# Kernel tuning notes

Hardware: AMD Instinct MI355X
Metric: run time of the kernel (lower is better)

The kernel has to match this reference:

```python
import jax, jax.numpy as jnp
import numpy as np

# ---- config (mirrors cfg / init kwargs) ----
FEAT_STRIDE = 16
IM_DIMS = (1024, 1024)          # (height, width)
ANCHOR_SCALES = (8, 16, 32)
ANCHOR_RATIOS = (0.5, 1.0, 2.0)
PRE_NMS_TOPN = 6000             # eval mode (cfg_key=1)
POST_NMS_TOPN = 300
NMS_THRESH = 0.7
MIN_SIZE = 16


def _generate_base_anchors(base_size=16, ratios=ANCHOR_RATIOS, scales=ANCHOR_SCALES):
    """py-faster-rcnn generate_anchors, in numpy (static)."""
    def mk(ws, hs, xc, yc):
        return np.stack([xc - 0.5 * (ws - 1), yc - 0.5 * (hs - 1),
                         xc + 0.5 * (ws - 1), yc + 0.5 * (hs - 1)], axis=1)
    base = np.array([0, 0, base_size - 1, base_size - 1], dtype=np.float64)
    w = base[2] - base[0] + 1; h = base[3] - base[1] + 1
    xc = base[0] + 0.5 * (w - 1); yc = base[1] + 0.5 * (h - 1)
    # ratio enum
    size = w * h
    ws = np.round(np.sqrt(size / np.array(ratios)))
    hs = np.round(ws * np.array(ratios))
    ratio_anchors = mk(ws, hs, xc, yc)
    # scale enum
    out = []
    for a in ratio_anchors:
        aw = a[2] - a[0] + 1; ah = a[3] - a[1] + 1
        axc = a[0] + 0.5 * (aw - 1); ayc = a[1] + 0.5 * (ah - 1)
        out.append(mk(aw * np.array(scales), ah * np.array(scales), axc, ayc))
    return np.concatenate(out, axis=0).astype(np.float32)  # [A,4]


def _all_anchors(H, W):
    base = _generate_base_anchors()                       # [A,4]
    sx = np.arange(W) * FEAT_STRIDE
    sy = np.arange(H) * FEAT_STRIDE
    sx, sy = np.meshgrid(sx, sy)
    shifts = np.stack([sx.ravel(), sy.ravel(), sx.ravel(), sy.ravel()], axis=1)  # [H*W,4]
    anchors = shifts[:, None, :].astype(np.float32) + base[None, :, :]
    return anchors.reshape(-1, 4)                         # [H*W*A, 4]


def setup_inputs() -> dict:
    key = jax.random.key(0)
    k1, k2 = jax.random.split(key)
    H, W, A = 64, 64, 9
    rpn_cls_score = jax.random.normal(k1, (1, H, W, 2 * A), dtype=jnp.float32)
    rpn_bbox_pred = jax.random.normal(k2, (1, H, W, 4 * A), dtype=jnp.float32)
    return {"rpn_cls_score": rpn_cls_score, "rpn_bbox_pred": rpn_bbox_pred}


def _proposals(rpn_cls_score, rpn_bbox_pred):
    _, H, W, C2 = rpn_cls_score.shape
    A = C2 // 2
    # rpn_softmax: per-anchor 2-way softmax, foreground prob
    scores = jax.nn.softmax(rpn_cls_score.reshape(H, W, A, 2), axis=-1)[..., 1].reshape(-1)  # [N]
    deltas = rpn_bbox_pred.reshape(-1, 4)                  # [N,4]
    anchors = jnp.asarray(_all_anchors(H, W))              # [N,4]
    # bbox_transform_inv
    aw = anchors[:, 2] - anchors[:, 0] + 1.0
    ah = anchors[:, 3] - anchors[:, 1] + 1.0
    axc = anchors[:, 0] + 0.5 * aw
    ayc = anchors[:, 1] + 0.5 * ah
    dx, dy, dw, dh = deltas[:, 0], deltas[:, 1], deltas[:, 2], deltas[:, 3]
    pxc = dx * aw + axc; pyc = dy * ah + ayc
    pw = jnp.exp(dw) * aw; ph = jnp.exp(dh) * ah
    x1 = pxc - 0.5 * pw; y1 = pyc - 0.5 * ph
    x2 = pxc + 0.5 * pw; y2 = pyc + 0.5 * ph
    # clip to image
    im_h, im_w = IM_DIMS
    x1 = jnp.clip(x1, 0.0, im_w - 1.0); x2 = jnp.clip(x2, 0.0, im_w - 1.0)
    y1 = jnp.clip(y1, 0.0, im_h - 1.0); y2 = jnp.clip(y2, 0.0, im_h - 1.0)
    boxes = jnp.stack([x1, y1, x2, y2], axis=1)            # [N,4]
    # filter too-small boxes by masking their score
    valid = ((x2 - x1 + 1.0) >= MIN_SIZE) & ((y2 - y1 + 1.0) >= MIN_SIZE)
    scores = jnp.where(valid, scores, -jnp.inf)
    return boxes, scores


def _nms_keep(boxes, K):
    """Greedy NMS keep-mask over score-descending boxes [K,4]."""
    x1, y1, x2, y2 = boxes[:, 0], boxes[:, 1], boxes[:, 2], boxes[:, 3]
    areas = (x2 - x1 + 1.0) * (y2 - y1 + 1.0)
    ix1 = jnp.maximum(x1[:, None], x1[None, :])
    iy1 = jnp.maximum(y1[:, None], y1[None, :])
    ix2 = jnp.minimum(x2[:, None], x2[None, :])
    iy2 = jnp.minimum(y2[:, None], y2[None, :])
    iw = jnp.maximum(ix2 - ix1 + 1.0, 0.0)
    ih = jnp.maximum(iy2 - iy1 + 1.0, 0.0)
    inter = iw * ih
    iou = inter / (areas[:, None] + areas[None, :] - inter)  # [K,K]
    idxs = jnp.arange(K)
    def body(i, keep):
        sup = keep[i] & (iou[i] > NMS_THRESH) & (idxs > i)
        return keep & ~sup
    return jax.lax.fori_loop(0, K, body, jnp.ones((K,), bool))


def reference(rpn_cls_score, rpn_bbox_pred):
    boxes, scores = _proposals(rpn_cls_score, rpn_bbox_pred)
    K = min(PRE_NMS_TOPN, scores.shape[0])
    top_scores, order = jax.lax.top_k(scores, K)           # score-descending
    top_boxes = boxes[order]                               # [K,4]
    keep = _nms_keep(top_boxes, K)
    sel_scores = jnp.where(keep, top_scores, -jnp.inf)
    _, idx = jax.lax.top_k(sel_scores, POST_NMS_TOPN)      # kept, in score order
    out_boxes = top_boxes[idx]                             # [post,4]
    blob = jnp.concatenate([jnp.zeros((POST_NMS_TOPN, 1), out_boxes.dtype), out_boxes], axis=1)
    return blob                                            # [post,5] (batch_idx, x1,y1,x2,y2)
```

## Files before the change

kernel.cpp:

```cpp
#include <hip/hip_runtime.h>
#include <stdint.h>

typedef unsigned long long u64;
typedef unsigned int u32;

#define N_ANCH 36864
#define WGRID 64
#define A_PER 9
#define KTOP 6000
#define NOUT 300
#define NBIN 5120
#define NCHK 94
#define NJ   6016
#define NSLOT 12
#define SPILLCAP 64
#define SCAP 6144

#define BARRIER_LDS() do {                                   \
    asm volatile("s_waitcnt lgkmcnt(0)" ::: "memory");       \
    __builtin_amdgcn_s_barrier();                            \
    asm volatile("" ::: "memory");                           \
} while (0)

__constant__ float c_ax1[9] = {-84.f,-176.f,-360.f,-56.f,-120.f,-248.f,-36.f,-80.f,-168.f};
__constant__ float c_ay1[9] = {-40.f,-88.f,-184.f,-56.f,-120.f,-248.f,-80.f,-168.f,-344.f};
__constant__ float c_aw[9]  = {184.f,368.f,736.f,128.f,256.f,512.f,88.f,176.f,352.f};
__constant__ float c_ah[9]  = {96.f,192.f,384.f,128.f,256.f,512.f,176.f,352.f,704.f};

__device__ __forceinline__ u32 binof(u32 u) {
    if (u < 0x80000000u) return 0u;
    if (u < 0xBF000000u) return 1u + ((u - 0x80000000u) >> 22);
    return 256u + ((u - 0xBF000000u) >> 11);
}

__device__ __forceinline__ bool iou_gt(float4 a, float areaA, float4 b, float areaB) {
    float ix1 = fmaxf(a.x, b.x), iy1 = fmaxf(a.y, b.y);
    float ix2 = fminf(a.z, b.z), iy2 = fminf(a.w, b.w);
    float iw = fmaxf(ix2 - ix1 + 1.0f, 0.0f);
    float ih = fmaxf(iy2 - iy1 + 1.0f, 0.0f);
    float inter = iw * ih;
    float iou = inter / (areaA + areaB - inter);
    return iou > 0.7f;
}

__global__ __launch_bounds__(256) void proposal_kernel(const float* __restrict__ cls,
                                                       const float* __restrict__ dlt,
                                                       u64* __restrict__ keys,
                                                       float4* __restrict__ boxes) {
    const int t = threadIdx.x;
    int i = blockIdx.x * 256 + t;
    int a  = i % A_PER;
    int hw = i / A_PER;
    int wx = hw % WGRID;
    int hy = hw / WGRID;

    float2 lp = *(const float2*)(cls + hw * 18 + 2 * a);
    float l0 = lp.x, l1 = lp.y;
    float m  = fmaxf(l0, l1);
    float e0 = expf(l0 - m), e1 = expf(l1 - m);
    float s  = e1 / (e0 + e1);

    float4 dd = *(const float4*)(dlt + hw * 36 + 4 * a);
    float dx = dd.x, dy = dd.y, dw = dd.z, dh = dd.w;
    float aw = c_aw[a], ah = c_ah[a];
    float axc = (c_ax1[a] + 16.f * (float)wx) + 0.5f * aw;
    float ayc = (c_ay1[a] + 16.f * (float)hy) + 0.5f * ah;

    float pxc = dx * aw + axc;
    float pyc = dy * ah + ayc;
    float pw  = expf(dw) * aw;
    float phh = expf(dh) * ah;
    float x1 = pxc - 0.5f * pw, y1 = pyc - 0.5f * phh;
    float x2 = pxc + 0.5f * pw, y2 = pyc + 0.5f * phh;
    x1 = fminf(fmaxf(x1, 0.f), 1023.f);
    x2 = fminf(fmaxf(x2, 0.f), 1023.f);
    y1 = fminf(fmaxf(y1, 0.f), 1023.f);
    y2 = fminf(fmaxf(y2, 0.f), 1023.f);
    bool valid = ((x2 - x1 + 1.f) >= 16.f) && ((y2 - y1 + 1.f) >= 16.f);
    float sc = valid ? s : -__builtin_huge_valf();

    u32 sb  = __float_as_uint(sc);
    u32 ord = (sb & 0x80000000u) ? ~sb : (sb | 0x80000000u);
    u64 key = ((u64)ord << 32) | (u32)(~(u32)i);
    keys[i]  = key;
    boxes[i] = make_float4(x1, y1, x2, y2);
}

__global__ __launch_bounds__(1024) void select_kernel(const u64* __restrict__ keys,
                                                      const float4* __restrict__ boxes,
                                                      u64* __restrict__ gscat,
                                                      float4* __restrict__ topBoxes,
                                                      u32* __restrict__ gEV) {
    __shared__ u32 lh[NBIN];
    __shared__ u32 bst[NBIN];
    __shared__ u64 scat[SCAP];
    __shared__ u32 wsum[16];
    __shared__ int sE;
    __shared__ int sV;
    const int t = threadIdx.x;
    const int lane = t & 63;
    const int v = t >> 6;
    for (int b = t; b < NBIN; b += 1024) lh[b] = 0;
    if (t == 0) { sV = KTOP; sE = KTOP; }
    __syncthreads();
    for (int i = t; i < N_ANCH; i += 1024) {
        u32 hiw = (u32)(keys[i] >> 32);
        atomicAdd(&lh[binof(hiw)], 1u);
    }
    __syncthreads();
    int hi = NBIN - 1 - 5 * t;
    u32 cnt[5];
    u32 sum = 0;
#pragma unroll
    for (int k = 0; k < 5; ++k) { cnt[k] = lh[hi - k]; sum += cnt[k]; }
    u32 s = sum;
#pragma unroll
    for (int d = 1; d < 64; d <<= 1) {
        u32 x = __shfl_up(s, d, 64);
        if (lane >= d) s += x;
    }
    if (lane == 63) wsum[v] = s;
    __syncthreads();
    u32 base = 0;
#pragma unroll
    for (int q = 0; q < 16; ++q) { u32 x = wsum[q]; if (q < v) base += x; }
    u32 run = base + s - sum;
#pragma unroll
    for (int k = 0; k < 5; ++k) {
        int b = hi - k;
        bst[b] = run;
        lh[b] = 0;
        u32 end = run + cnt[k];
        if (run < KTOP && end >= KTOP) sE = (int)end;
        run = end;
    }
    __syncthreads();
    for (int i = t; i < N_ANCH; i += 1024) {
        u64 k = keys[i];
        u32 b = binof((u32)(k >> 32));
        u32 s0 = bst[b];
        if (s0 < KTOP) {
            u32 p = s0 + atomicAdd(&lh[b], 1u);
            if (p < SCAP) scat[p] = k; else gscat[p] = k;
        }
    }
    __syncthreads();
    const int E = sE;
    for (int i = t; i < E; i += 1024) {
        u64 k = (i < SCAP) ? scat[i] : gscat[i];
        u32 b = binof((u32)(k >> 32));
        u32 s0 = bst[b];
        u32 e0 = (b > 0) ? bst[b - 1] : (u32)N_ANCH;
        u32 r = s0;
        for (u32 j = s0; j < e0; ++j) {
            u64 kj = (j < SCAP) ? scat[j] : gscat[j];
            r += (kj > k) ? 1u : 0u;
        }
        if (r < KTOP) {
            int idx = (int)(~(u32)k);
            topBoxes[r] = boxes[idx];
            if (!(k >> 63)) atomicMin(&sV, (int)r);
        }
    }
    __syncthreads();
    if (t == 0) gEV[1] = (u32)sV;
}

__global__ __launch_bounds__(256) void maskT_kernel(const float4* __restrict__ topBoxes,
                                                    const u32* __restrict__ gEV,
                                                    u64* __restrict__ S) {
    const int V = (int)gEV[1];
    const int nch = (V + 63) >> 6;
    const int ntask = nch * (nch + 1) / 2;
    const int lane = threadIdx.x & 63;
    const int v = threadIdx.x >> 6;
    for (int tk = blockIdx.x * 4 + v; tk < ntask; tk += gridDim.x * 4) {
        int jc = (int)((sqrtf(8.f * (float)tk + 1.f) - 1.f) * 0.5f);
        while ((jc + 1) * (jc + 2) / 2 <= tk) ++jc;
        while (jc * (jc + 1) / 2 > tk) --jc;
        int w = tk - jc * (jc + 1) / 2;
        int ci = w * 64 + lane;
        float4 bi = (ci < V) ? topBoxes[ci] : make_float4(0.f, 0.f, -8.f, -8.f);
        float ai = (bi.z - bi.x + 1.f) * (bi.w - bi.y + 1.f);
        int j = jc * 64 + lane;
        float4 bj = (j < V) ? topBoxes[j] : make_float4(0.f, 0.f, -8.f, -8.f);
        float aj = (bj.z - bj.x + 1.f) * (bj.w - bj.y + 1.f);
        u64 m = 0;
#pragma unroll 4
        for (int b = 0; b < 64; ++b) {
            float4 bb;
            bb.x = __shfl(bi.x, b, 64); bb.y = __shfl(bi.y, b, 64);
            bb.z = __shfl(bi.z, b, 64); bb.w = __shfl(bi.w, b, 64);
            float ab = __shfl(ai, b, 64);
            if (iou_gt(bb, ab, bj, aj)) m |= (1ull << b);
        }
        if (w == jc) m &= ((1ull << lane) - 1ull);
        S[(u64)w * NJ + j] = m;
    }
}

#define SLOT_DECL(K) u64 kw##K = 0, pa##K = 0, pb##K = 0; u32 ao##K = 0;
#define SLOT_ACC(K)  if (nslot > 4*(K) + v) { accA |= pa##K & kw##K; accB |= pb##K & kw##K; }
#define SLOT_REF(K)  if (nslot > 4*(K) + v) { const u64* rp_ = S + (u64)ao##K * NJ + ofsn; pa##K = rp_[0]; pb##K = rp_[64]; }
#define SLOT_CASE(K) case K: kw##K = kb_; ao##K = wch_; if (pf_) { const u64* rp_ = S + (u64)wch_ * NJ + onx_; pa##K = rp_[0]; pb##K = rp_[64]; } break;
#define DO_CLAIM(KB, WCH) do {                                                \
    u64 kb_ = (KB); u32 wch_ = (WCH);                                         \
    int si_ = nslot >> 2, so_ = nslot & 3;                                    \
    if (si_ < NSLOT) {                                                        \
      if (v == so_) {                                                         \
        bool pf_ = (r + 1 < nr);                                              \
        u64 onx_ = (u64)(128 * (r + 1)) + lane;                               \
        switch (si_) {                                                        \
          SLOT_CASE(0) SLOT_CASE(1) SLOT_CASE(2) SLOT_CASE(3)                 \
          SLOT_CASE(4) SLOT_CASE(5) SLOT_CASE(6) SLOT_CASE(7)                 \
          SLOT_CASE(8) SLOT_CASE(9) SLOT_CASE(10) SLOT_CASE(11)               \
          default: break;                                                     \
        }                                                                     \
      }                                                                       \
      ++nslot;                                                                \
    } else if (nspill < SPILLCAP) {                                           \
      if (v == 3 && lane == 0) { spillW[nspill] = wch_; spillK[nspill] = kb_; } \
      ++nspill; sadd = true;                                                  \
    }                                                                         \
  } while (0)

__global__ __launch_bounds__(256, 1) void nms_out_kernel(const float4* __restrict__ topBoxes,
                                                         const u32* __restrict__ gEV,
                                                         const u64* __restrict__ S,
                                                         float* __restrict__ out) {
    __shared__ u64 keepw[NCHK];
    __shared__ u64 supw[2][8];
    __shared__ u64 spillK[SPILLCAP];
    __shared__ u32 spillW[SPILLCAP];
    __shared__ u32 wsum[4];
    const int t = threadIdx.x;
    const int lane = t & 63;
    const int v = t >> 6;
    const int V = (int)gEV[1];
    const int nch = (V + 63) >> 6;
    const int nr  = (nch + 1) >> 1;
    if (t < NCHK) keepw[t] = 0;

    SLOT_DECL(0) SLOT_DECL(1) SLOT_DECL(2) SLOT_DECL(3)
    SLOT_DECL(4) SLOT_DECL(5) SLOT_DECL(6) SLOT_DECL(7)
    SLOT_DECL(8) SLOT_DECL(9) SLOT_DECL(10) SLOT_DECL(11)

    u64 dAc  = S[lane];
    u64 dABc = S[64 + lane];
    u64 dBc  = S[(u64)NJ + 64 + lane];
    int nslot = 0, nspill = 0, nkept = 0;

    for (int r = 0; r < nr; ++r) {
        const int par = r & 1;
        u64 accA = 0, accB = 0;
        SLOT_ACC(0) SLOT_ACC(1) SLOT_ACC(2) SLOT_ACC(3)
        SLOT_ACC(4) SLOT_ACC(5) SLOT_ACC(6) SLOT_ACC(7)
        SLOT_ACC(8) SLOT_ACC(9) SLOT_ACC(10) SLOT_ACC(11)
        for (int s2 = v; s2 < nspill; s2 += 4) {
            u64 kk = spillK[s2];
            const u64* row = S + (u64)spillW[s2] * NJ + 128 * r + lane;
            accA |= row[0] & kk; accB |= row[64] & kk;
        }
        u64 bA = __ballot(accA != 0ull), bB = __ballot(accB != 0ull);
        if (lane == 0) { supw[par][v] = bA; supw[par][4 + v] = bB; }
        u64 dAn = 0, dABn = 0, dBn = 0;
        if (r + 1 < nr) {
            u64 ofsn = (u64)(128 * (r + 1)) + lane;
            SLOT_REF(0) SLOT_REF(1) SLOT_REF(2) SLOT_REF(3)
            SLOT_REF(4) SLOT_REF(5) SLOT_REF(6) SLOT_REF(7)
            SLOT_REF(8) SLOT_REF(9) SLOT_REF(10) SLOT_REF(11)
            int rn = r + 1;
            dAn  = S[(u64)(2 * rn) * NJ + 128 * rn + lane];
            dABn = S[(u64)(2 * rn) * NJ + 128 * rn + 64 + lane];
            dBn  = S[(u64)(2 * rn + 1) * NJ + 128 * rn + 64 + lane];
        }
        BARRIER_LDS();
        u64 rwA = supw[par][0] | supw[par][1] | supw[par][2] | supw[par][3];
        u64 rwB = supw[par][4] | supw[par][5] | supw[par][6] | supw[par][7];
        int remA = V - 128 * r;
        int remB = remA - 64;
        u64 aliveA = (remA >= 64) ? ~0ull : ((remA <= 0) ? 0ull : ((1ull << remA) - 1ull));
        u64 aliveB = (remB >= 64) ? ~0ull : ((remB <= 0) ? 0ull : ((1ull << remB) - 1ull));
        u64 candA = ~rwA & aliveA, kbA = 0;
        while (candA) {
            int b = __builtin_ctzll(candA);
            kbA |= (1ull << b);
            candA &= ~(1ull << b);
            candA &= ~__ballot(((dAc >> b) & 1ull) != 0ull);
        }
        u64 supAB = __ballot((dABc & kbA) != 0ull);
        u64 candB = ~(rwB | supAB) & aliveB, kbB = 0;
        while (candB) {
            int b = __builtin_ctzll(candB);
            kbB |= (1ull << b);
            candB &= ~(1ull << b);
            candB &= ~__ballot(((dBc >> b) & 1ull) != 0ull);
        }
        if (t == 0) { keepw[2 * r] = kbA; if (2 * r + 1 < nch) keepw[2 * r + 1] = kbB; }
        bool sadd = false;
        if (kbA) DO_CLAIM(kbA, (u32)(2 * r));
        if (kbB) DO_CLAIM(kbB, (u32)(2 * r + 1));
        if (sadd) BARRIER_LDS();
        nkept += __popcll(kbA) + __popcll(kbB);
        dAc = dAn; dABc = dABn; dBc = dBn;
        if (nkept >= NOUT) break;
    }
    __syncthreads();

    const int per = 24;
    int r0 = t * per;
    int r1 = min(r0 + per, KTOP);
    u32 cnt2 = 0;
    for (int rr = r0; rr < r1; ++rr)
        cnt2 += (u32)((keepw[rr >> 6] >> (rr & 63)) & 1ull);
    u32 s2 = cnt2;
#pragma unroll
    for (int d = 1; d < 64; d <<= 1) {
        u32 x = __shfl_up(s2, d, 64);
        if (lane >= d) s2 += x;
    }
    if (lane == 63) wsum[v] = s2;
    __syncthreads();
    u32 base = 0, total = 0;
#pragma unroll
    for (int q = 0; q < 4; ++q) {
        u32 x = wsum[q];
        if (q < v) base += x;
        total += x;
    }
    const int n1 = min((int)total, NOUT);
    int kp = (int)(base + s2 - cnt2);
    for (int rr = r0; rr < r1; ++rr) {
        int kept = (int)((keepw[rr >> 6] >> (rr & 63)) & 1ull);
        int pos = kept ? kp : (n1 + rr - kp);
        if (pos < NOUT) {
            float4 b = topBoxes[rr];
            out[pos * 5 + 0] = 0.f;
            out[pos * 5 + 1] = b.x; out[pos * 5 + 2] = b.y;
            out[pos * 5 + 3] = b.z; out[pos * 5 + 4] = b.w;
        }
        kp += kept;
    }
}

extern "C" void kernel_launch(void* const* d_in, const int* in_sizes, int n_in,
                              void* d_out, int out_size, void* d_ws, size_t ws_size,
                              hipStream_t stream) {
    const float* cls = (const float*)d_in[0];
    const float* dlt = (const float*)d_in[1];
    float* out = (float*)d_out;
    char* ws = (char*)d_ws;
    u64*    keys     = (u64*)   (ws);
    u64*    gscat    = (u64*)   (ws + 294912);
    float4* boxes    = (float4*)(ws + 589824);
    float4* topBoxes = (float4*)(ws + 1179648);
    u32*    gEV      = (u32*)   (ws + 1337088);
    u64*    S        = (u64*)   (ws + 1337344);

    proposal_kernel<<<144, 256, 0, stream>>>(cls, dlt, keys, boxes);
    select_kernel<<<1, 1024, 0, stream>>>(keys, boxes, gscat, topBoxes, gEV);
    maskT_kernel<<<1120, 256, 0, stream>>>(topBoxes, gEV, S);
    nms_out_kernel<<<1, 256, 0, stream>>>(topBoxes, gEV, S, out);
}
```

Before: 136.7 us.

## Build score histogram across proposal blocks instead of in single-block select kernel

Histogram construction over all anchor keys moves out of the single-workgroup select kernel into the 144-block proposal kernel. Each block builds a shared-memory histogram, collapsing invalid (-inf) scores into one ballot-based atomic, then flushes its nonzero bins to a global histogram with atomics. The select kernel then reads the finished histogram instead of rescanning all keys. This adds a memset launch, per-block zeroing and flushing of 5120 bins, and global atomic traffic in exchange for removing a serial pass from the one-block kernel.

```diff
diff --git a/kernel.cpp b/kernel.cpp
--- a/kernel.cpp
+++ b/kernel.cpp
@@ -46,8 +46,14 @@
 __global__ __launch_bounds__(256) void proposal_kernel(const float* __restrict__ cls,
                                                        const float* __restrict__ dlt,
                                                        u64* __restrict__ keys,
-                                                       float4* __restrict__ boxes) {
+                                                       float4* __restrict__ boxes,
+                                                       u32* __restrict__ hist) {
+    __shared__ u32 lh[NBIN];
     const int t = threadIdx.x;
+    const int lane = t & 63;
+    for (int b = t; b < NBIN; b += 256) lh[b] = 0;
+    __syncthreads();
+
     int i = blockIdx.x * 256 + t;
     int a  = i % A_PER;
     int hw = i / A_PER;
@@ -84,15 +90,29 @@
     u64 key = ((u64)ord << 32) | (u32)(~(u32)i);
     keys[i]  = key;
     boxes[i] = make_float4(x1, y1, x2, y2);
-}
-
-__global__ __launch_bounds__(1024) void select_kernel(const u64* __restrict__ keys,
+
+    u64 infb = __ballot(!valid);
+    if (valid) {
+        atomicAdd(&lh[binof(ord)], 1u);
+    } else {
+        if (lane == __builtin_ctzll(infb))
+            atomicAdd(&lh[0], (u32)__popcll(infb));
+    }
+    __syncthreads();
+    for (int b = t; b < NBIN; b += 256) {
+        u32 x = lh[b];
+        if (x) atomicAdd(&hist[b], x);
+    }
+}
+
+__global__ __launch_bounds__(1024) void select_kernel(const u32* __restrict__ hist,
+                                                      const u64* __restrict__ keys,
                                                       const float4* __restrict__ boxes,
                                                       u64* __restrict__ gscat,
                                                       float4* __restrict__ topBoxes,
                                                       u32* __restrict__ gEV) {
-    __shared__ u32 lh[NBIN];
     __shared__ u32 bst[NBIN];
+    __shared__ u32 cur[NBIN];
     __shared__ u64 scat[SCAP];
     __shared__ u32 wsum[16];
     __shared__ int sE;
@@ -100,19 +120,12 @@
     const int t = threadIdx.x;
     const int lane = t & 63;
     const int v = t >> 6;
-    for (int b = t; b < NBIN; b += 1024) lh[b] = 0;
     if (t == 0) { sV = KTOP; sE = KTOP; }
-    __syncthreads();
-    for (int i = t; i < N_ANCH; i += 1024) {
-        u32 hiw = (u32)(keys[i] >> 32);
-        atomicAdd(&lh[binof(hiw)], 1u);
-    }
-    __syncthreads();
     int hi = NBIN - 1 - 5 * t;
     u32 cnt[5];
     u32 sum = 0;
 #pragma unroll
-    for (int k = 0; k < 5; ++k) { cnt[k] = lh[hi - k]; sum += cnt[k]; }
+    for (int k = 0; k < 5; ++k) { cnt[k] = hist[hi - k]; sum += cnt[k]; }
     u32 s = sum;
 #pragma unroll
     for (int d = 1; d < 64; d <<= 1) {
@@ -129,7 +142,7 @@
     for (int k = 0; k < 5; ++k) {
         int b = hi - k;
         bst[b] = run;
-        lh[b] = 0;
+        cur[b] = 0;
         u32 end = run + cnt[k];
         if (run < KTOP && end >= KTOP) sE = (int)end;
         run = end;
@@ -140,7 +153,7 @@
         u32 b = binof((u32)(k >> 32));
         u32 s0 = bst[b];
         if (s0 < KTOP) {
-            u32 p = s0 + atomicAdd(&lh[b], 1u);
+            u32 p = s0 + atomicAdd(&cur[b], 1u);
             if (p < SCAP) scat[p] = k; else gscat[p] = k;
         }
     }
@@ -354,11 +367,13 @@
     u64*    gscat    = (u64*)   (ws + 294912);
     float4* boxes    = (float4*)(ws + 589824);
     float4* topBoxes = (float4*)(ws + 1179648);
+    u32*    hist     = (u32*)   (ws + 1275648);
     u32*    gEV      = (u32*)   (ws + 1337088);
     u64*    S        = (u64*)   (ws + 1337344);
 
-    proposal_kernel<<<144, 256, 0, stream>>>(cls, dlt, keys, boxes);
-    select_kernel<<<1, 1024, 0, stream>>>(keys, boxes, gscat, topBoxes, gEV);
+    hipMemsetAsync(hist, 0, NBIN * sizeof(u32), stream);
+    proposal_kernel<<<144, 256, 0, stream>>>(cls, dlt, keys, boxes, hist);
+    select_kernel<<<1, 1024, 0, stream>>>(hist, keys, boxes, gscat, topBoxes, gEV);
     maskT_kernel<<<1120, 256, 0, stream>>>(topBoxes, gEV, S);
     nms_out_kernel<<<1, 256, 0, stream>>>(topBoxes, gEV, S, out);
 }
```

New measurement: 134.6 us. About the same (-1.5%).
